# Optimization experiments

Hardware: AMD Instinct MI355X
Metric: run time of the kernel (lower is better)

## Reference

```python
import jax, jax.numpy as jnp
import numpy as np

B, T, S, D, H, F = 4, 1024, 1024, 1024, 16, 4096
NEG = jnp.float32(-1e9)


def _ln(x, g, b):
    m = jnp.mean(x, axis=-1, keepdims=True)
    v = jnp.mean((x - m) ** 2, axis=-1, keepdims=True)
    return (x - m) * jax.lax.rsqrt(v + 1e-5) * g + b


def _mha(q, k, v, wq, bq, wk, bk, wv, bv, wo, bo, scale, mask, causal, sbias):
    Bq, Tq, Dq = q.shape
    Sk = k.shape[1]
    dk = Dq // H
    Q = (q @ wq.T + bq).reshape(Bq, Tq, H, dk).transpose(0, 2, 1, 3)  # [B,H,T,dk]
    K = (k @ wk.T + bk).reshape(Bq, Sk, H, dk).transpose(0, 2, 1, 3)  # [B,H,S,dk]
    V = (v @ wv.T + bv).reshape(Bq, Sk, H, dk).transpose(0, 2, 1, 3)
    s = jnp.einsum('bhtd,bhsd->bhts', Q, K) / jnp.sqrt(jnp.float32(dk))
    if sbias is not None:
        s = s + scale * sbias[:, None, None, :]
    if mask is not None:
        s = jnp.where(mask == 0, NEG, s)
    if causal is not None:
        s = jnp.where(causal == 0, NEG, s)
    a = jax.nn.softmax(s, axis=-1)
    o = jnp.einsum('bhts,bhsd->bhtd', a, V).transpose(0, 2, 1, 3).reshape(Bq, Tq, Dq)
    return o @ wo.T + bo


def setup_inputs():
    key = jax.random.key(0)
    ks = jax.random.split(key, 16)
    r = lambda i, shape, s=0.02: jax.random.normal(ks[i], shape, dtype=jnp.float32) * s
    z = lambda *shape: jnp.zeros(shape, jnp.float32)
    o = lambda *shape: jnp.ones(shape, jnp.float32)
    inp = dict(
        x=r(0, (B, T, D), 1.0),
        memory=r(1, (B, S, D), 1.0),
        sentence_bias=r(2, (B, S), 1.0),
        trg_mask=jnp.ones((B, 1, 1, T), jnp.int32),
        trg_causal_mask=jnp.tril(jnp.ones((T, T), jnp.int32))[None, None],
        src_mask=jnp.ones((B, 1, 1, S), jnp.int32),
        sa_wq=r(3, (D, D)), sa_bq=z(D), sa_wk=r(4, (D, D)), sa_bk=z(D),
        sa_wv=r(5, (D, D)), sa_bv=z(D), sa_wo=r(6, (D, D)), sa_bo=z(D),
        sa_scale=jnp.float32(0.1),
        ca_wq=r(7, (D, D)), ca_bq=z(D), ca_wk=r(8, (D, D)), ca_bk=z(D),
        ca_wv=r(9, (D, D)), ca_bv=z(D), ca_wo=r(10, (D, D)), ca_bo=z(D),
        ca_scale=jnp.float32(0.1),
        ln1_g=o(D), ln1_b=z(D), ln2_g=o(D), ln2_b=z(D), ln3_g=o(D), ln3_b=z(D),
        ffn_w1=r(11, (F, D)), ffn_b1=z(F), ffn_w2=r(12, (D, F)), ffn_b2=z(D),
    )
    return inp


def reference(x, memory, trg_mask, trg_causal_mask, src_mask, sentence_bias,
              sa_wq, sa_bq, sa_wk, sa_bk, sa_wv, sa_bv, sa_wo, sa_bo, sa_scale,
              ca_wq, ca_bq, ca_wk, ca_bk, ca_wv, ca_bv, ca_wo, ca_bo, ca_scale,
              ln1_g, ln1_b, ln2_g, ln2_b, ln3_g, ln3_b,
              ffn_w1, ffn_b1, ffn_w2, ffn_b2):
    # Faithful quirk: Q comes from normed x, K/V from raw residual stream.
    x = x + _mha(_ln(x, ln1_g, ln1_b), x, x,
                 sa_wq, sa_bq, sa_wk, sa_bk, sa_wv, sa_bv, sa_wo, sa_bo,
                 sa_scale, trg_mask, trg_causal_mask, None)
    x = x + _mha(_ln(x, ln2_g, ln2_b), memory, memory,
                 ca_wq, ca_bq, ca_wk, ca_bk, ca_wv, ca_bv, ca_wo, ca_bo,
                 ca_scale, src_mask, None, sentence_bias)
    h = _ln(x, ln3_g, ln3_b)
    x = x + (jax.nn.relu(h @ ffn_w1.T + ffn_b1) @ ffn_w2.T + ffn_b2)
    return x
```

## Files before the change

### kernel.cpp

```cpp
#include <hip/hip_runtime.h>
#include <hip/hip_bf16.h>
#include <cmath>
#include <stdint.h>

typedef __hip_bfloat16 bf16;
typedef __attribute__((ext_vector_type(8))) __bf16 bf16x8;
typedef __attribute__((ext_vector_type(8))) unsigned short u16x8;
typedef __attribute__((ext_vector_type(4))) float f32x4;

__device__ __forceinline__ void gld16(const void* g, const void* l)
{
    __builtin_amdgcn_global_load_lds(
        (const __attribute__((address_space(1))) unsigned int*)(unsigned long long)g,
        (__attribute__((address_space(3))) unsigned int*)(unsigned int)(unsigned long long)l,
        16, 0, 0);
}

struct CvtSrcs { const float* p[24]; };

__global__ __launch_bounds__(256) void cvt_all(CvtSrcs s, bf16* __restrict__ dst)
{
    const int i = (blockIdx.x * 256 + threadIdx.x) * 8;
    const int seg = i >> 20;
    const float* sp = s.p[seg] + (i & 1048575);
    const float4 a = *(const float4*)(sp);
    const float4 b = *(const float4*)(sp + 4);
    const float v[8] = {a.x, a.y, a.z, a.w, b.x, b.y, b.z, b.w};
    bf16 tmp[8];
#pragma unroll
    for (int j = 0; j < 8; ++j) tmp[j] = __float2bfloat16(v[j]);
    *(uint4*)(dst + i) = *(const uint4*)tmp;
}

enum {
    EPI_QSCALE = 0,
    EPI_KV = 1,
    EPI_RELU = 2,
    EPI_RES_F32_F32OUT = 3,
    EPI_PART = 4
};

template <int EPI>
__global__ __launch_bounds__(512, 2) void gemm256(
    const bf16* __restrict__ A, const bf16* __restrict__ W,
    const float* __restrict__ bias, void* __restrict__ out,
    int N, int Kiter, int Kstride)
{
    __shared__ __align__(16) unsigned short sA[2][2][128 * 64];
    __shared__ __align__(16) unsigned short sB[2][2][128 * 64];

    const int t  = threadIdx.x;
    const int l  = t & 63;
    const int w  = t >> 6;
    const int wv = w * 64;
    const int wr = w >> 2;
    const int wc = w & 3;
    const int lm = l & 15;
    const int kq = l >> 4;
    const int rx = lm & 7;

    int bx = blockIdx.x;
    if (EPI == EPI_PART) {
        const int chunk = bx >> 6;
        bx &= 63;
        A += (size_t)chunk * 1024;
        W += (size_t)chunk * 1024;
        out = (void*)((bf16*)out + (size_t)chunk * 4096 * 1024);
    }
    const int xcd = bx & 7;
    const int ib  = bx >> 3;
    const int bm  = xcd * 2 + (ib & 1);
    const int bn  = ib >> 1;

    const bf16* gA = A + (size_t)(bm * 256 + (t >> 3)) * Kstride
                       + ((t & 7) ^ ((t >> 3) & 7)) * 8;
    const bf16* gB = W + (size_t)(bn * 256 + (t >> 3)) * Kstride
                       + ((t & 7) ^ ((t >> 3) & 7)) * 8;

#define SQA(slot, kt, j)                                        \
    gld16(gA + (size_t)((j) * 64) * Kstride + (kt) * 64,        \
          &sA[slot][(j) >> 1][(((j) & 1) * 512 + wv) * 8])
#define SQB(slot, kt, j)                                        \
    gld16(gB + (size_t)((j) * 64) * Kstride + (kt) * 64,        \
          &sB[slot][(j) >> 1][(((j) & 1) * 512 + wv) * 8])

    bf16x8 af[4][2], bg[2][2];

#define READ_AF(s_, mh)                                                     \
    do {                                                                    \
        _Pragma("unroll")                                                   \
        for (int mi = 0; mi < 4; ++mi)                                      \
            _Pragma("unroll")                                               \
            for (int kk = 0; kk < 2; ++kk) {                                \
                const int lr = (mh) * 64 + mi * 16 + lm;                    \
                const int sl = ((kk << 2) | kq) ^ rx;                       \
                af[mi][kk] = __builtin_bit_cast(bf16x8,                     \
                    *(const u16x8*)(&sA[s_][wr][lr * 64 + sl * 8]));        \
            }                                                               \
    } while (0)
#define READ_BG(s_, nh)                                                     \
    do {                                                                    \
        _Pragma("unroll")                                                   \
        for (int ni = 0; ni < 2; ++ni)                                      \
            _Pragma("unroll")                                               \
            for (int kk = 0; kk < 2; ++kk) {                                \
                const int lr = (wc & 1) * 64 + (nh) * 32 + ni * 16 + lm;    \
                const int sl = ((kk << 2) | kq) ^ rx;                       \
                bg[ni][kk] = __builtin_bit_cast(bf16x8,                     \
                    *(const u16x8*)(&sB[s_][wc >> 1][lr * 64 + sl * 8]));   \
            }                                                               \
    } while (0)
#define MFMA_QUAD(mh, nh)                                                   \
    do {                                                                    \
        __builtin_amdgcn_s_setprio(1);                                      \
        _Pragma("unroll")                                                   \
        for (int mi = 0; mi < 4; ++mi)                                      \
            _Pragma("unroll")                                               \
            for (int ni = 0; ni < 2; ++ni)                                  \
                _Pragma("unroll")                                           \
                for (int kk = 0; kk < 2; ++kk)                              \
                    acc[(mh) * 4 + mi][(nh) * 2 + ni] =                     \
                        __builtin_amdgcn_mfma_f32_16x16x32_bf16(            \
                            af[mi][kk], bg[ni][kk],                         \
                            acc[(mh) * 4 + mi][(nh) * 2 + ni], 0, 0, 0);    \
        __builtin_amdgcn_s_setprio(0);                                      \
    } while (0)
#define BARRIER() do { __builtin_amdgcn_s_barrier();                        \
                       __builtin_amdgcn_sched_barrier(0); } while (0)
#define WAITV4() asm volatile("s_waitcnt vmcnt(4)" ::: "memory")
#define WAITV2() asm volatile("s_waitcnt vmcnt(2)" ::: "memory")
#define WAITV0() asm volatile("s_waitcnt vmcnt(0)" ::: "memory")

    f32x4 acc[8][4] = {};
    const int NT = Kiter >> 6;

    SQB(0, 0, 0); SQB(0, 0, 1); SQB(0, 0, 2); SQB(0, 0, 3);
    SQA(0, 0, 0); SQA(0, 0, 2); SQA(0, 0, 1); SQA(0, 0, 3);

    for (int tt = 0; tt < NT - 1; ++tt) {
        const int s = tt & 1, d = s ^ 1, kn = tt + 1;
        WAITV2(); BARRIER();
        SQB(d, kn, 0); SQB(d, kn, 1);
        READ_AF(s, 0); READ_BG(s, 0);
        MFMA_QUAD(0, 0);
        WAITV2(); BARRIER();
        SQB(d, kn, 2); SQB(d, kn, 3);
        READ_AF(s, 1);
        MFMA_QUAD(1, 0);
        SQA(d, kn, 0); SQA(d, kn, 2);
        READ_BG(s, 1);
        MFMA_QUAD(1, 1);
        SQA(d, kn, 1); SQA(d, kn, 3);
        READ_AF(s, 0);
        MFMA_QUAD(0, 1);
    }
    {
        const int s = (NT - 1) & 1;
        WAITV2(); BARRIER();
        READ_AF(s, 0); READ_BG(s, 0);
        MFMA_QUAD(0, 0);
        WAITV0(); BARRIER();
        READ_AF(s, 1);
        MFMA_QUAD(1, 0);
        READ_BG(s, 1);
        MFMA_QUAD(1, 1);
        READ_AF(s, 0);
        MFMA_QUAD(0, 1);
    }

    __syncthreads();
    unsigned short* scr = (w < 4) ? &sA[0][0][0] + w * 8192
                                  : &sB[0][0][0] + (w - 4) * 8192;

#pragma unroll
    for (int NI = 0; NI < 4; ++NI) {
        const int col = bn * 256 + wc * 64 + NI * 16 + lm;
        const float bv = (EPI == EPI_PART) ? 0.f : bias[col];
        const int c  = NI * 2 + (lm >> 3);
        const int ci = lm & 7;
#pragma unroll
        for (int MI = 0; MI < 8; ++MI) {
#pragma unroll
            for (int r = 0; r < 4; ++r) {
                float v = acc[MI][NI][r] + bv;
                if (EPI == EPI_RELU) v = fmaxf(v, 0.f);
                const int row = MI * 16 + kq * 4 + r;
                scr[row * 64 + ((c ^ (row & 7)) * 8) + ci] =
                    __builtin_bit_cast(unsigned short, (__bf16)v);
            }
        }
    }
#pragma unroll
    for (int it = 0; it < 16; ++it) {
        const int row = it * 8 + (l >> 3);
        const int lc  = l & 7;
        const u16x8 vv = *(const u16x8*)&scr[row * 64 + ((lc ^ (row & 7)) * 8)];
        const int Crow = bm * 256 + wr * 128 + row;
        const int Ccol = bn * 256 + wc * 64 + lc * 8;
        *(u16x8*)((bf16*)out + (size_t)Crow * N + Ccol) = vv;
    }
#undef SQA
#undef SQB
#undef READ_AF
#undef READ_BG
#undef MFMA_QUAD
}

template <int EPI>
__global__ __launch_bounds__(256, 2) void gemm_bt(
    const bf16* __restrict__ A, const bf16* __restrict__ W,
    const float* __restrict__ bias, const float* __restrict__ bias2,
    const float* __restrict__ res, void* __restrict__ out,
    int M, int N, int Kiter, int Kstride)
{
    __shared__ __align__(16) unsigned short sA[2][128 * 64];
    __shared__ __align__(16) unsigned short sB[2][128 * 64];

    const int t  = threadIdx.x;
    const int l  = t & 63;
    const int w  = t >> 6;
    const int wv = w * 64;
    const int wm = (w >> 1) * 64;
    const int wn = (w & 1) * 64;
    const int lm = l & 15;
    const int kq = l >> 4;
    const int rx = lm & 7;

    const int bx  = blockIdx.x;
    const int xcd = bx & 7;
    const int ib  = bx >> 3;
    const int bm  = xcd * 4 + (ib & 3);
    const int bn  = ib >> 2;

    const bf16* gA = A + (size_t)(bm * 128 + (t >> 3)) * Kstride
                       + ((t & 7) ^ ((t >> 3) & 7)) * 8;
    const bf16* gB = W + (size_t)(bn * 128 + (t >> 3)) * Kstride
                       + ((t & 7) ^ ((t >> 3) & 7)) * 8;

#define SQA(slot, kt, j)                                        \
    gld16(gA + (size_t)((j) * 32) * Kstride + (kt) * 64,        \
          &sA[slot][((j) * 256 + wv) * 8])
#define SQB(slot, kt, j)                                        \
    gld16(gB + (size_t)((j) * 32) * Kstride + (kt) * 64,        \
          &sB[slot][((j) * 256 + wv) * 8])

    bf16x8 af[2][2], bg[2][2];

#define READ_AF(s_, mh)                                                     \
    do {                                                                    \
        _Pragma("unroll")                                                   \
        for (int mi = 0; mi < 2; ++mi)                                      \
            _Pragma("unroll")                                               \
            for (int kk = 0; kk < 2; ++kk) {                                \
                const int lr = wm + (mh) * 32 + mi * 16 + lm;               \
                const int sl = ((kk << 2) | kq) ^ rx;                       \
                af[mi][kk] = __builtin_bit_cast(bf16x8,                     \
                    *(const u16x8*)(&sA[s_][lr * 64 + sl * 8]));            \
            }                                                               \
    } while (0)
#define READ_BG(s_, nh)                                                     \
    do {                                                                    \
        _Pragma("unroll")                                                   \
        for (int ni = 0; ni < 2; ++ni)                                      \
            _Pragma("unroll")                                               \
            for (int kk = 0; kk < 2; ++kk) {                                \
                const int lr = wn + (nh) * 32 + ni * 16 + lm;               \
                const int sl = ((kk << 2) | kq) ^ rx;                       \
                bg[ni][kk] = __builtin_bit_cast(bf16x8,                     \
                    *(const u16x8*)(&sB[s_][lr * 64 + sl * 8]));            \
            }                                                               \
    } while (0)
#define MFMA_QUAD(mh, nh)                                                   \
    do {                                                                    \
        __builtin_amdgcn_s_setprio(1);                                      \
        _Pragma("unroll")                                                   \
        for (int mi = 0; mi < 2; ++mi)                                      \
            _Pragma("unroll")                                               \
            for (int ni = 0; ni < 2; ++ni)                                  \
                _Pragma("unroll")                                           \
                for (int kk = 0; kk < 2; ++kk)                              \
                    acc[(mh) * 2 + mi][(nh) * 2 + ni] =                     \
                        __builtin_amdgcn_mfma_f32_16x16x32_bf16(            \
                            af[mi][kk], bg[ni][kk],                         \
                            acc[(mh) * 2 + mi][(nh) * 2 + ni], 0, 0, 0);    \
        __builtin_amdgcn_s_setprio(0);                                      \
    } while (0)

    f32x4 acc[4][4] = {};
    const int NT = Kiter >> 6;

    SQB(0, 0, 0); SQB(0, 0, 2); SQA(0, 0, 0); SQA(0, 0, 2);
    SQB(0, 0, 1); SQB(0, 0, 3); SQA(0, 0, 1); SQA(0, 0, 3);

    for (int tt = 0; tt < NT - 1; ++tt) {
        const int s = tt & 1, d = s ^ 1, kn = tt + 1;
        WAITV4(); BARRIER();
        SQB(d, kn, 0); SQB(d, kn, 2);
        READ_AF(s, 0); READ_BG(s, 0);
        MFMA_QUAD(0, 0);
        WAITV2(); BARRIER();
        SQA(d, kn, 0); SQA(d, kn, 2);
        READ_AF(s, 1);
        MFMA_QUAD(1, 0);
        SQB(d, kn, 1); SQB(d, kn, 3);
        READ_BG(s, 1);
        MFMA_QUAD(1, 1);
        SQA(d, kn, 1); SQA(d, kn, 3);
        READ_AF(s, 0);
        MFMA_QUAD(0, 1);
    }
    {
        const int s = (NT - 1) & 1;
        WAITV4(); BARRIER();
        READ_AF(s, 0); READ_BG(s, 0);
        MFMA_QUAD(0, 0);
        WAITV0(); BARRIER();
        READ_AF(s, 1);
        MFMA_QUAD(1, 0);
        READ_BG(s, 1);
        MFMA_QUAD(1, 1);
        READ_AF(s, 0);
        MFMA_QUAD(0, 1);
    }
#undef SQA
#undef SQB
#undef READ_AF
#undef READ_BG
#undef MFMA_QUAD
#undef BARRIER
#undef WAITV4
#undef WAITV2
#undef WAITV0

#pragma unroll
    for (int ni = 0; ni < 4; ++ni) {
        const int col = bn * 128 + wn + ni * 16 + lm;
        float bv = 0.f;
        if (EPI == EPI_KV) bv = (col < 1024) ? bias[col] : bias2[col - 1024];
        else bv = bias[col];
#pragma unroll
        for (int mi = 0; mi < 4; ++mi) {
#pragma unroll
            for (int r = 0; r < 4; ++r) {
                const int row = bm * 128 + wm + mi * 16 + kq * 4 + r;
                float v = acc[mi][ni][r] + bv;
                if (EPI == EPI_QSCALE) v *= 0.125f;
                if (EPI == EPI_KV) {
                    if (col < 1024) {
                        ((bf16*)out)[(size_t)row * 1024 + col] = __float2bfloat16(v);
                    } else {
                        const int ch = col - 1024;
                        const size_t idx = (size_t)4 * 1048576 +
                            ((size_t)((row >> 10) * 16 + (ch >> 6)) * 64 + (ch & 63)) * 1024
                            + (row & 1023);
                        ((bf16*)out)[idx] = __float2bfloat16(v);
                    }
                } else if (EPI == EPI_RES_F32_F32OUT) {
                    const size_t idx = (size_t)row * N + col;
                    ((float*)out)[idx] = v + res[idx];
                } else {
                    ((bf16*)out)[(size_t)row * N + col] = __float2bfloat16(v);
                }
            }
        }
    }
}

__global__ __launch_bounds__(256) void ffn2_reduce(
    const bf16* __restrict__ P, const float* __restrict__ x2,
    const float* __restrict__ b2, float* __restrict__ out)
{
    const int i = (blockIdx.x * 256 + threadIdx.x) * 8;
    float v[8];
    {
        const float4 a = *(const float4*)(x2 + i);
        const float4 b = *(const float4*)(x2 + i + 4);
        v[0]=a.x; v[1]=a.y; v[2]=a.z; v[3]=a.w; v[4]=b.x; v[5]=b.y; v[6]=b.z; v[7]=b.w;
    }
    const int cb = i & 1023;
#pragma unroll
    for (int j = 0; j < 8; ++j) v[j] += b2[cb + j];
#pragma unroll
    for (int c = 0; c < 4; ++c) {
        const u16x8 u = *(const u16x8*)(P + (size_t)c * 4194304 + i);
        const bf16x8 pb = __builtin_bit_cast(bf16x8, u);
#pragma unroll
        for (int j = 0; j < 8; ++j) v[j] += (float)pb[j];
    }
    float4 o0 = {v[0], v[1], v[2], v[3]}, o1 = {v[4], v[5], v[6], v[7]};
    *(float4*)(out + i) = o0;
    *(float4*)(out + i + 4) = o1;
}

template <bool CAUSAL, bool SBIAS>
__global__ __launch_bounds__(256, 2) void flash_attn(
    const bf16* __restrict__ Q, const bf16* __restrict__ K,
    const bf16* __restrict__ Vt, bf16* __restrict__ O,
    const float* __restrict__ sbias, const float* __restrict__ scale_ptr)
{
    __shared__ __align__(16) unsigned short sK[2][64 * 64];
    __shared__ __align__(16) unsigned short sV[2][64 * 64];
    __shared__ __align__(16) unsigned short sP[4 * 32 * 72];

    const int t  = threadIdx.x;
    const int l  = t & 63;
    const int w  = t >> 6;
    const int wv = w * 64;
    const int lm = l & 15;
    const int kq = l >> 4;

    const int bh = blockIdx.x & 63;
    const int qb = blockIdx.x >> 6;
    const int h  = bh & 15;
    const int b  = bh >> 4;

    const int tb = qb * 128 + w * 32;
    const size_t qrow0 = (size_t)(b * 1024 + tb) * 1024 + h * 64;

    bf16x8 qf[2][2];
#pragma unroll
    for (int mi = 0; mi < 2; ++mi)
#pragma unroll
        for (int kk = 0; kk < 2; ++kk)
            qf[mi][kk] = __builtin_bit_cast(bf16x8,
                *(const u16x8*)(Q + qrow0 + (size_t)(mi * 16 + lm) * 1024 + kk * 32 + kq * 8));

    float cs = 0.f; const float* sb = nullptr;
    if (SBIAS) { cs = scale_ptr[0]; sb = sbias + b * 1024; }

    const bf16* gK = K  + (size_t)(b * 1024 + (t >> 3)) * 1024 + h * 64
                   + ((t & 7) ^ ((t >> 3) & 7)) * 8;
    const bf16* gV = Vt + (size_t)((b * 16 + h) * 64 + (t >> 3)) * 1024
                   + ((t & 7) ^ ((t >> 3) & 7)) * 8;
    __bf16* sPw = (__bf16*)sP + w * 32 * 72;

#define STAGE_KV(buf, s0r)                                                   \
    do {                                                                     \
        gld16(gK + (size_t)(s0r) * 1024,        &sK[buf][wv * 8]);           \
        gld16(gK + (size_t)((s0r) + 32) * 1024, &sK[buf][2048 + wv * 8]);    \
        gld16(gV + (s0r),                       &sV[buf][wv * 8]);           \
        gld16(gV + (s0r) + 32 * 1024,           &sV[buf][2048 + wv * 8]);    \
    } while (0)

    const int niter = CAUSAL ? (2 * qb + 2) : 16;

    STAGE_KV(0, 0);
    __syncthreads();

    f32x4 acc_o[2][4] = {};
    f32x4 l_run[2] = {};

    for (int it = 0; it < niter; ++it) {
        const int s0 = it * 64;
        const int cur = it & 1;

        if (it + 1 < niter) STAGE_KV(cur ^ 1, s0 + 64);

        f32x4 accs[2][4] = {};
#pragma unroll
        for (int ni = 0; ni < 4; ++ni)
#pragma unroll
            for (int kk = 0; kk < 2; ++kk) {
                const bf16x8 kf = __builtin_bit_cast(bf16x8,
                    *(const u16x8*)(&sK[cur][(ni * 16 + lm) * 64
                        + ((((kk << 2) | kq)) ^ (lm & 7)) * 8]));
#pragma unroll
                for (int mi = 0; mi < 2; ++mi)
                    accs[mi][ni] = __builtin_amdgcn_mfma_f32_16x16x32_bf16(
                        qf[mi][kk], kf, accs[mi][ni], 0, 0, 0);
            }

        if (SBIAS) {
#pragma unroll
            for (int ni = 0; ni < 4; ++ni) {
                const float sv = cs * sb[s0 + ni * 16 + lm];
#pragma unroll
                for (int mi = 0; mi < 2; ++mi)
#pragma unroll
                    for (int r = 0; r < 4; ++r) accs[mi][ni][r] += sv;
            }
        }
        if (CAUSAL && (s0 + 63 > tb)) {
#pragma unroll
            for (int ni = 0; ni < 4; ++ni) {
                const int s = s0 + ni * 16 + lm;
#pragma unroll
                for (int mi = 0; mi < 2; ++mi)
#pragma unroll
                    for (int r = 0; r < 4; ++r)
                        if (s > tb + mi * 16 + kq * 4 + r) accs[mi][ni][r] = -1e30f;
            }
        }

#pragma unroll
        for (int mi = 0; mi < 2; ++mi)
#pragma unroll
            for (int ni = 0; ni < 4; ++ni)
#pragma unroll
                for (int r = 0; r < 4; ++r) {
                    const float e = __expf(accs[mi][ni][r]);
                    l_run[mi][r] += e;
                    sPw[(mi * 16 + kq * 4 + r) * 72 + ni * 16 + lm] = (__bf16)e;
                }

#pragma unroll
        for (int kk = 0; kk < 2; ++kk) {
            bf16x8 pf[2];
#pragma unroll
            for (int mi = 0; mi < 2; ++mi)
                pf[mi] = __builtin_bit_cast(bf16x8,
                    *(const u16x8*)(sPw + (mi * 16 + lm) * 72 + kk * 32 + kq * 8));
#pragma unroll
            for (int di = 0; di < 4; ++di) {
                const bf16x8 vf = __builtin_bit_cast(bf16x8,
                    *(const u16x8*)(&sV[cur][(di * 16 + lm) * 64
                        + ((((kk << 2) | kq)) ^ (lm & 7)) * 8]));
#pragma unroll
                for (int mi = 0; mi < 2; ++mi)
                    acc_o[mi][di] = __builtin_amdgcn_mfma_f32_16x16x32_bf16(
                        pf[mi], vf, acc_o[mi][di], 0, 0, 0);
            }
        }

        __syncthreads();
    }
#undef STAGE_KV

#pragma unroll
    for (int mi = 0; mi < 2; ++mi) {
        f32x4 lt = l_run[mi];
#pragma unroll
        for (int x = 1; x < 16; x <<= 1)
#pragma unroll
            for (int r = 0; r < 4; ++r) lt[r] += __shfl_xor(lt[r], x, 64);
#pragma unroll
        for (int r = 0; r < 4; ++r) lt[r] = 1.f / lt[r];
#pragma unroll
        for (int di = 0; di < 4; ++di)
#pragma unroll
            for (int r = 0; r < 4; ++r) {
                const size_t idx = (size_t)(b * 1024 + tb + mi * 16 + kq * 4 + r) * 1024
                                 + h * 64 + di * 16 + lm;
                O[idx] = __float2bfloat16(acc_o[mi][di][r] * lt[r]);
            }
    }
}

__global__ __launch_bounds__(256) void ln_kernel(
    const float* __restrict__ xin, const float* __restrict__ g,
    const float* __restrict__ bta, bf16* __restrict__ out)
{
    const int row = blockIdx.x;
    const int t = threadIdx.x;
    const size_t base = (size_t)row * 1024 + t * 4;

    const float4 f = *(const float4*)(xin + base);
    const float v[4] = {f.x, f.y, f.z, f.w};
    float s1 = v[0] + v[1] + v[2] + v[3];
    float s2 = v[0]*v[0] + v[1]*v[1] + v[2]*v[2] + v[3]*v[3];
#pragma unroll
    for (int off = 32; off > 0; off >>= 1) {
        s1 += __shfl_xor(s1, off, 64);
        s2 += __shfl_xor(s2, off, 64);
    }
    __shared__ float r1[4], r2[4];
    if ((t & 63) == 0) { r1[t >> 6] = s1; r2[t >> 6] = s2; }
    __syncthreads();
    s1 = r1[0] + r1[1] + r1[2] + r1[3];
    s2 = r2[0] + r2[1] + r2[2] + r2[3];
    const float mean = s1 * (1.f / 1024.f);
    const float var  = s2 * (1.f / 1024.f) - mean * mean;
    const float rstd = rsqrtf(var + 1e-5f);
#pragma unroll
    for (int j = 0; j < 4; ++j) {
        const int c = t * 4 + j;
        out[base + j] = __float2bfloat16((v[j] - mean) * rstd * g[c] + bta[c]);
    }
}

extern "C" void kernel_launch(void* const* d_in, const int* in_sizes, int n_in,
                              void* d_out, int out_size, void* d_ws, size_t ws_size,
                              hipStream_t stream)
{
    const float* x       = (const float*)d_in[0];
    const float* memory  = (const float*)d_in[1];
    const float* sbias   = (const float*)d_in[2];
    const float* sa_bq = (const float*)d_in[7];
    const float* sa_bk = (const float*)d_in[9];
    const float* sa_bv = (const float*)d_in[11];
    const float* sa_bo = (const float*)d_in[13];
    const float* ca_bq = (const float*)d_in[16];
    const float* ca_bk = (const float*)d_in[18];
    const float* ca_bv = (const float*)d_in[20];
    const float* ca_bo = (const float*)d_in[22];
    const float* ca_scale = (const float*)d_in[23];
    const float* ln1_g = (const float*)d_in[24]; const float* ln1_b = (const float*)d_in[25];
    const float* ln2_g = (const float*)d_in[26]; const float* ln2_b = (const float*)d_in[27];
    const float* ln3_g = (const float*)d_in[28]; const float* ln3_b = (const float*)d_in[29];
    const float* b1 = (const float*)d_in[31];
    const float* b2 = (const float*)d_in[33];

    char* ws = (char*)d_ws;
    const size_t MB = (size_t)1 << 20;
    float* x1    = (float*)(ws + 0 * MB);
    float* x2    = (float*)(ws + 16 * MB);
    bf16* lnbuf  = (bf16*)(ws + 32 * MB);
    bf16* Qb     = (bf16*)(ws + 40 * MB);
    bf16* Kb     = (bf16*)(ws + 48 * MB);
    bf16* Vtb    = (bf16*)(ws + 56 * MB);
    bf16* Ob     = (bf16*)(ws + 64 * MB);
    bf16* ffnmid = (bf16*)(ws + 40 * MB);
    bf16* wx     = (bf16*)(ws + 72 * MB);
    bf16* wmem   = (bf16*)(ws + 80 * MB);
    bf16* bw     = (bf16*)(ws + 88 * MB);
    bf16* b_sa_wq = bw + 0 * 1048576, *b_sa_wk = bw + 1 * 1048576;
    bf16* b_sa_wo = bw + 3 * 1048576;
    bf16* b_ca_wq = bw + 4 * 1048576, *b_ca_wk = bw + 5 * 1048576;
    bf16* b_ca_wo = bw + 7 * 1048576;
    bf16* b_w1   = (bf16*)(ws + 104 * MB);
    bf16* b_w2   = (bf16*)(ws + 112 * MB);
    bf16* part   = (bf16*)(ws + 72 * MB);

    const int M = 4096;
    dim3 blk256(256), blk512(512);
    const dim3 gQ(256);
    const dim3 gKV(512);
    const dim3 gFA(512);
    const dim3 g256(256);

    CvtSrcs cs;
    for (int c = 0; c < 4; ++c) {
        cs.p[c]      = x + (size_t)c * 1048576;
        cs.p[4 + c]  = memory + (size_t)c * 1048576;
        cs.p[16 + c] = (const float*)d_in[30] + (size_t)c * 1048576;
        cs.p[20 + c] = (const float*)d_in[32] + (size_t)c * 1048576;
    }
    cs.p[8]  = (const float*)d_in[6];
    cs.p[9]  = (const float*)d_in[8];
    cs.p[10] = (const float*)d_in[10];
    cs.p[11] = (const float*)d_in[12];
    cs.p[12] = (const float*)d_in[15];
    cs.p[13] = (const float*)d_in[17];
    cs.p[14] = (const float*)d_in[19];
    cs.p[15] = (const float*)d_in[21];
    cvt_all<<<24 * 1048576 / 2048, blk256, 0, stream>>>(cs, wx);

    ln_kernel<<<4096, blk256, 0, stream>>>(x, ln1_g, ln1_b, lnbuf);
    gemm_bt<EPI_QSCALE><<<gQ, blk256, 0, stream>>>(
        lnbuf, b_sa_wq, sa_bq, nullptr, nullptr, Qb, M, 1024, 1024, 1024);
    gemm_bt<EPI_KV><<<gKV, blk256, 0, stream>>>(
        wx, b_sa_wk, sa_bk, sa_bv, nullptr, Kb, M, 2048, 1024, 1024);
    flash_attn<true, false><<<gFA, blk256, 0, stream>>>(Qb, Kb, Vtb, Ob, nullptr, nullptr);
    gemm_bt<EPI_RES_F32_F32OUT><<<gQ, blk256, 0, stream>>>(
        Ob, b_sa_wo, sa_bo, nullptr, x, x1, M, 1024, 1024, 1024);

    ln_kernel<<<4096, blk256, 0, stream>>>(x1, ln2_g, ln2_b, lnbuf);
    gemm_bt<EPI_QSCALE><<<gQ, blk256, 0, stream>>>(
        lnbuf, b_ca_wq, ca_bq, nullptr, nullptr, Qb, M, 1024, 1024, 1024);
    gemm_bt<EPI_KV><<<gKV, blk256, 0, stream>>>(
        wmem, b_ca_wk, ca_bk, ca_bv, nullptr, Kb, M, 2048, 1024, 1024);
    flash_attn<false, true><<<gFA, blk256, 0, stream>>>(Qb, Kb, Vtb, Ob, sbias, ca_scale);
    gemm_bt<EPI_RES_F32_F32OUT><<<gQ, blk256, 0, stream>>>(
        Ob, b_ca_wo, ca_bo, nullptr, x1, x2, M, 1024, 1024, 1024);

    ln_kernel<<<4096, blk256, 0, stream>>>(x2, ln3_g, ln3_b, lnbuf);
    gemm256<EPI_RELU><<<g256, blk512, 0, stream>>>(
        lnbuf, b_w1, b1, ffnmid, 4096, 1024, 1024);
    gemm256<EPI_PART><<<g256, blk512, 0, stream>>>(
        ffnmid, b_w2, nullptr, part, 1024, 1024, 4096);
    ffn2_reduce<<<2048, blk256, 0, stream>>>(part, x2, b2, (float*)d_out);
}
```

Baseline: 478.1 us.

## Fuse LN1 into conversion kernel and replace split-K FFN2 with direct GEMM

```diff
diff --git a/kernel.cpp b/kernel.cpp
--- a/kernel.cpp
+++ b/kernel.cpp
@@ -18,9 +18,13 @@
 
 struct CvtSrcs { const float* p[24]; };
 
-__global__ __launch_bounds__(256) void cvt_all(CvtSrcs s, bf16* __restrict__ dst)
+__global__ __launch_bounds__(256) void cvt_all(
+    CvtSrcs s, bf16* __restrict__ dst,
+    const float* __restrict__ lg, const float* __restrict__ lb,
+    bf16* __restrict__ lnout)
 {
-    const int i = (blockIdx.x * 256 + threadIdx.x) * 8;
+    const int t = threadIdx.x;
+    const int i = (blockIdx.x * 256 + t) * 8;
     const int seg = i >> 20;
     const float* sp = s.p[seg] + (i & 1048575);
     const float4 a = *(const float4*)(sp);
@@ -30,6 +34,33 @@
 #pragma unroll
     for (int j = 0; j < 8; ++j) tmp[j] = __float2bfloat16(v[j]);
     *(uint4*)(dst + i) = *(const uint4*)tmp;
+
+    if (seg < 4) {
+        float s1 = 0.f, s2 = 0.f;
+#pragma unroll
+        for (int j = 0; j < 8; ++j) { s1 += v[j]; s2 += v[j] * v[j]; }
+#pragma unroll
+        for (int off = 32; off > 0; off >>= 1) {
+            s1 += __shfl_xor(s1, off, 64);
+            s2 += __shfl_xor(s2, off, 64);
+        }
+        __shared__ float r1[4], r2[4];
+        const int w = t >> 6;
+        if ((t & 63) == 0) { r1[w] = s1; r2[w] = s2; }
+        __syncthreads();
+        const int rw = (w >> 1) * 2;
+        s1 = r1[rw] + r1[rw + 1];
+        s2 = r2[rw] + r2[rw + 1];
+        const float mean = s1 * (1.f / 1024.f);
+        const float var  = s2 * (1.f / 1024.f) - mean * mean;
+        const float rstd = rsqrtf(var + 1e-5f);
+        bf16 lt[8];
+        const int c0 = i & 1023;
+#pragma unroll
+        for (int j = 0; j < 8; ++j)
+            lt[j] = __float2bfloat16((v[j] - mean) * rstd * lg[c0 + j] + lb[c0 + j]);
+        *(uint4*)(lnout + i) = *(const uint4*)lt;
+    }
 }
 
 enum {
@@ -60,13 +91,6 @@
     const int rx = lm & 7;
 
     int bx = blockIdx.x;
-    if (EPI == EPI_PART) {
-        const int chunk = bx >> 6;
-        bx &= 63;
-        A += (size_t)chunk * 1024;
-        W += (size_t)chunk * 1024;
-        out = (void*)((bf16*)out + (size_t)chunk * 4096 * 1024);
-    }
     const int xcd = bx & 7;
     const int ib  = bx >> 3;
     const int bm  = xcd * 2 + (ib & 1);
@@ -175,7 +199,7 @@
 #pragma unroll
     for (int NI = 0; NI < 4; ++NI) {
         const int col = bn * 256 + wc * 64 + NI * 16 + lm;
-        const float bv = (EPI == EPI_PART) ? 0.f : bias[col];
+        const float bv = bias[col];
         const int c  = NI * 2 + (lm >> 3);
         const int ci = lm & 7;
 #pragma unroll
@@ -366,32 +390,6 @@
     }
 }
 
-__global__ __launch_bounds__(256) void ffn2_reduce(
-    const bf16* __restrict__ P, const float* __restrict__ x2,
-    const float* __restrict__ b2, float* __restrict__ out)
-{
-    const int i = (blockIdx.x * 256 + threadIdx.x) * 8;
-    float v[8];
-    {
-        const float4 a = *(const float4*)(x2 + i);
-        const float4 b = *(const float4*)(x2 + i + 4);
-        v[0]=a.x; v[1]=a.y; v[2]=a.z; v[3]=a.w; v[4]=b.x; v[5]=b.y; v[6]=b.z; v[7]=b.w;
-    }
-    const int cb = i & 1023;
-#pragma unroll
-    for (int j = 0; j < 8; ++j) v[j] += b2[cb + j];
-#pragma unroll
-    for (int c = 0; c < 4; ++c) {
-        const u16x8 u = *(const u16x8*)(P + (size_t)c * 4194304 + i);
-        const bf16x8 pb = __builtin_bit_cast(bf16x8, u);
-#pragma unroll
-        for (int j = 0; j < 8; ++j) v[j] += (float)pb[j];
-    }
-    float4 o0 = {v[0], v[1], v[2], v[3]}, o1 = {v[4], v[5], v[6], v[7]};
-    *(float4*)(out + i) = o0;
-    *(float4*)(out + i + 4) = o1;
-}
-
 template <bool CAUSAL, bool SBIAS>
 __global__ __launch_bounds__(256, 2) void flash_attn(
     const bf16* __restrict__ Q, const bf16* __restrict__ K,
@@ -619,7 +617,6 @@
     bf16* b_ca_wo = bw + 7 * 1048576;
     bf16* b_w1   = (bf16*)(ws + 104 * MB);
     bf16* b_w2   = (bf16*)(ws + 112 * MB);
-    bf16* part   = (bf16*)(ws + 72 * MB);
 
     const int M = 4096;
     dim3 blk256(256), blk512(512);
@@ -643,9 +640,9 @@
     cs.p[13] = (const float*)d_in[17];
     cs.p[14] = (const float*)d_in[19];
     cs.p[15] = (const float*)d_in[21];
-    cvt_all<<<24 * 1048576 / 2048, blk256, 0, stream>>>(cs, wx);
-
-    ln_kernel<<<4096, blk256, 0, stream>>>(x, ln1_g, ln1_b, lnbuf);
+    cvt_all<<<24 * 1048576 / 2048, blk256, 0, stream>>>(
+        cs, wx, ln1_g, ln1_b, lnbuf);
+
     gemm_bt<EPI_QSCALE><<<gQ, blk256, 0, stream>>>(
         lnbuf, b_sa_wq, sa_bq, nullptr, nullptr, Qb, M, 1024, 1024, 1024);
     gemm_bt<EPI_KV><<<gKV, blk256, 0, stream>>>(
@@ -666,7 +663,6 @@
     ln_kernel<<<4096, blk256, 0, stream>>>(x2, ln3_g, ln3_b, lnbuf);
     gemm256<EPI_RELU><<<g256, blk512, 0, stream>>>(
         lnbuf, b_w1, b1, ffnmid, 4096, 1024, 1024);
-    gemm256<EPI_PART><<<g256, blk512, 0, stream>>>(
-        ffnmid, b_w2, nullptr, part, 1024, 1024, 4096);
-    ffn2_reduce<<<2048, blk256, 0, stream>>>(part, x2, b2, (float*)d_out);
+    gemm_bt<EPI_RES_F32_F32OUT><<<gQ, blk256, 0, stream>>>(
+        ffnmid, b_w2, b2, nullptr, x2, d_out, M, 1024, 4096, 4096);
 }
```

Result: faster. 457.6 us (-4.3%).
